# Kernel optimization log

Measured on AMD Instinct MI355X. Metric: run time of the kernel, lower is better.

## Reference

```python
import jax, jax.numpy as jnp
import numpy as np

DIM = 768
HEADS = 12
HIDDEN = 4 * DIM
EPS = 1e-5


def _layernorm(x, g, b):
    mu = jnp.mean(x, axis=-1, keepdims=True)
    var = jnp.var(x, axis=-1, keepdims=True)
    return (x - mu) * jax.lax.rsqrt(var + EPS) * g + b


def setup_inputs() -> dict:
    key = jax.random.key(0)
    ks = jax.random.split(key, 8)
    B, N, C = 16, 577, DIM
    s = lambda fan: 1.0 / np.sqrt(fan)
    return {
        "x": jax.random.normal(ks[0], (B, N, C), jnp.float32),
        "ln1_g": jnp.ones((C,), jnp.float32),
        "ln1_b": jnp.zeros((C,), jnp.float32),
        "qkv_w": jax.random.normal(ks[1], (C, 3 * C), jnp.float32) * s(C),
        "qkv_b": jnp.zeros((3 * C,), jnp.float32),
        "proj_w": jax.random.normal(ks[2], (C, C), jnp.float32) * s(C),
        "proj_b": jnp.zeros((C,), jnp.float32),
        "ln2_g": jnp.ones((C,), jnp.float32),
        "ln2_b": jnp.zeros((C,), jnp.float32),
        "fc1_w": jax.random.normal(ks[3], (C, HIDDEN), jnp.float32) * s(C),
        "fc1_b": jnp.zeros((HIDDEN,), jnp.float32),
        "fc2_w": jax.random.normal(ks[4], (HIDDEN, C), jnp.float32) * s(HIDDEN),
        "fc2_b": jnp.zeros((C,), jnp.float32),
    }


def reference(x, ln1_g, ln1_b, qkv_w, qkv_b, proj_w, proj_b,
              ln2_g, ln2_b, fc1_w, fc1_b, fc2_w, fc2_b):
    B, N, C = x.shape
    H = HEADS
    Dh = C // H
    scale = Dh ** (-0.5)

    # --- attention branch (pre-norm) ---
    xn = _layernorm(x, ln1_g, ln1_b)
    qkv = xn @ qkv_w + qkv_b                         # [B,N,3C]
    qkv = qkv.reshape(B, N, 3, H, Dh).transpose(2, 0, 3, 1, 4)  # [3,B,H,N,Dh]
    q, k, v = qkv[0], qkv[1], qkv[2]
    attn = jax.nn.softmax(jnp.einsum('bhnd,bhmd->bhnm', q, k) * scale, axis=-1)
    y = jnp.einsum('bhnm,bhmd->bhnd', attn, v)       # [B,H,N,Dh]
    y = y.transpose(0, 2, 1, 3).reshape(B, N, C)
    y = y @ proj_w + proj_b
    x = x + y

    # --- MLP branch (pre-norm, exact GELU as torch default) ---
    xn2 = _layernorm(x, ln2_g, ln2_b)
    h = jax.nn.gelu(xn2 @ fc1_w + fc1_b, approximate=False)
    x = x + (h @ fc2_w + fc2_b)
    return x
```

## Files before the change

### kernel.cpp

```cpp
#include <hip/hip_runtime.h>
#include <hip/hip_bf16.h>
#include <math.h>


#define C_DIM   768
#define SEQ     577
#define BATCH   16
#define NHEAD   12
#define DHEAD   64
#define MREAL   (BATCH*SEQ)
#define MPAD    9344
#define HID     3072
#define QKW     1536
#define NKV     640
#define QSCALE  0.1803368801111204f

typedef __hip_bfloat16 bf16;
typedef __attribute__((ext_vector_type(8))) short v8s;
typedef __attribute__((ext_vector_type(4))) float v4f;

static __device__ __forceinline__ bf16 f2b(float f){ return __float2bfloat16(f); }
static __device__ __forceinline__ float us2f(unsigned short u){
  union{ float f; unsigned int i; } x; x.i = ((unsigned int)u)<<16; return x.f;
}
static __device__ __forceinline__ short f2s(float f){
  bf16 t = __float2bfloat16(f); return *(short*)&t;
}
static __device__ __forceinline__ float gelu_fast(float x){
  float z2 = 2.302585092994046f * x * (1.f + 0.044715f*x*x);
  return x / (1.f + exp2f(-z2));
}


__global__ __launch_bounds__(256) void k_transpose_cast(
    const float* __restrict__ src, bf16* __restrict__ dst, int R, int C)
{
  __shared__ float s[64][65];
  const int tr = blockIdx.x*64, tc = blockIdx.y*64;
  const int t = threadIdx.x;
  const int lr = t >> 4, lc4 = t & 15;
  #pragma unroll
  for (int i=0;i<4;i++){
    int r = lr + i*16;
    float4 v = *(const float4*)(src + (size_t)(tr+r)*C + tc + lc4*4);
    s[r][lc4*4+0]=v.x; s[r][lc4*4+1]=v.y; s[r][lc4*4+2]=v.z; s[r][lc4*4+3]=v.w;
  }
  __syncthreads();
  const int c = t >> 2, seg = t & 3;
  alignas(16) bf16 tmp[16];
  #pragma unroll
  for (int j=0;j<16;j++) tmp[j] = f2b(s[seg*16+j][c]);
  bf16* dp = dst + (size_t)(tc+c)*R + tr + seg*16;
  *(uint4*)dp       = *(uint4*)tmp;
  *(uint4*)(dp + 8) = *(uint4*)(tmp + 8);
}

__global__ __launch_bounds__(256) void k_zero_pad(bf16* __restrict__ y)
{
  size_t i = (size_t)blockIdx.x*256 + threadIdx.x;
  y[(size_t)MREAL*C_DIM + i] = f2b(0.f);
}

__global__ __launch_bounds__(256) void k_layernorm(
    const float* __restrict__ in, const float* __restrict__ g,
    const float* __restrict__ b, bf16* __restrict__ o)
{
  int row = blockIdx.x, tid = threadIdx.x;
  size_t base = (size_t)row*C_DIM;
  if (row >= MREAL){
    #pragma unroll
    for (int j=0;j<3;j++) o[base + tid + j*256] = f2b(0.f);
    return;
  }
  float v[3], s=0.f, ss=0.f;
  #pragma unroll
  for (int j=0;j<3;j++){ v[j] = in[base + tid + j*256]; s += v[j]; ss += v[j]*v[j]; }
  #pragma unroll
  for (int off=32; off>0; off>>=1){ s += __shfl_xor(s,off); ss += __shfl_xor(ss,off); }
  __shared__ float red[8];
  int wv = tid>>6;
  if ((tid&63)==0){ red[wv] = s; red[4+wv] = ss; }
  __syncthreads();
  float S  = red[0]+red[1]+red[2]+red[3];
  float SS = red[4]+red[5]+red[6]+red[7];
  float mu   = S*(1.f/C_DIM);
  float rstd = rsqrtf(SS*(1.f/C_DIM) - mu*mu + 1e-5f);
  #pragma unroll
  for (int j=0;j<3;j++){
    int c = tid + j*256;
    o[base+c] = f2b((v[j]-mu)*rstd*g[c] + b[c]);
  }
}

__global__ __launch_bounds__(256) void k_reduce2(
    const bf16* __restrict__ P, const float* __restrict__ bias,
    float* __restrict__ out)
{
  size_t i = ((size_t)blockIdx.x*256 + threadIdx.x)*8;
  int c = (int)(i % C_DIM);
  v8s p0 = *(const v8s*)(P + i);
  v8s p1 = *(const v8s*)(P + (size_t)MPAD*C_DIM + i);
  float r[8];
  #pragma unroll
  for (int j=0;j<8;j++) r[j] = out[i+j];
  #pragma unroll
  for (int j=0;j<8;j++)
    out[i+j] = us2f((unsigned short)p0[j]) + us2f((unsigned short)p1[j])
             + bias[c+j] + r[j];
}

__global__ __launch_bounds__(256, 3) void k_flash(
    const bf16* __restrict__ qk, const bf16* __restrict__ VtAll,
    bf16* __restrict__ y)
{
  __shared__ alignas(16) bf16 sK[2][64*64];
  __shared__ alignas(16) bf16 sV[2][64*64];
  __shared__ alignas(16) bf16 sP[4][16*72];

  const int tid = threadIdx.x;
  const int wave = tid>>6, lane = tid&63;
  const int r16 = lane&15, kg = lane>>4;

  const int id = blockIdx.x;
  const int swz = (id&7)*240 + (id>>3);
  const int hh = swz/10, qt = swz - hh*10;
  const int b_ = hh/NHEAD, h_ = hh - b_*NHEAD;

  const int qrow = b_*SEQ + qt*64 + wave*16 + r16;
  v8s qf[2];
  qf[0] = *(const v8s*)(qk + (size_t)qrow*QKW + h_*DHEAD + kg*8);
  qf[1] = *(const v8s*)(qk + (size_t)qrow*QKW + h_*DHEAD + 32 + kg*8);

  auto stage = [&](int kt, int buf){
    #pragma unroll
    for (int i=0;i<2;i++){
      int chunk = i*256 + tid;
      int row = chunk>>3, ch = chunk&7;
      int sc = ch ^ (row&7);
      const bf16* gk = qk + (size_t)(b_*SEQ + kt*64 + row)*QKW
                          + C_DIM + h_*DHEAD + sc*8;
      const bf16* gv = VtAll + (size_t)(b_*C_DIM + h_*DHEAD + row)*NKV
                             + kt*64 + sc*8;
      __builtin_amdgcn_global_load_lds(
          (const __attribute__((address_space(1))) void*)gk,
          (__attribute__((address_space(3))) void*)((char*)&sK[buf][0] + i*4096 + wave*1024),
          16, 0, 0);
      __builtin_amdgcn_global_load_lds(
          (const __attribute__((address_space(1))) void*)gv,
          (__attribute__((address_space(3))) void*)((char*)&sV[buf][0] + i*4096 + wave*1024),
          16, 0, 0);
    }
  };

  float m_run = -1e30f, l_run = 0.f;
  v4f zero4 = {0.f,0.f,0.f,0.f};
  v4f o[4] = {zero4, zero4, zero4, zero4};

  stage(0, 0);
  for (int kt=0; kt<10; ++kt){
    __syncthreads();
    if (kt < 9) stage(kt+1, (kt+1)&1);
    const bf16* Kt = &sK[kt&1][0];
    const bf16* Vt = &sV[kt&1][0];

    v4f sfr[4] = {zero4, zero4, zero4, zero4};
    #pragma unroll
    for (int ks=0; ks<2; ++ks){
      #pragma unroll
      for (int m=0;m<4;m++){
        int key = m*16 + r16;
        v8s kf = *(const v8s*)(Kt + key*64 + (((ks*4+kg) ^ (key&7))*8));
        sfr[m] = __builtin_amdgcn_mfma_f32_16x16x32_bf16(kf, qf[ks], sfr[m], 0, 0, 0);
      }
    }

    if (kt == 9){
      #pragma unroll
      for (int m=0;m<4;m++)
        #pragma unroll
        for (int gg=0; gg<4; ++gg){
          int kb = 576 + m*16 + kg*4 + gg;
          if (kb >= SEQ) sfr[m][gg] = -1e30f;
        }
    }

    float tmax = -1e30f;
    #pragma unroll
    for (int m=0;m<4;m++)
      #pragma unroll
      for (int gg=0; gg<4; ++gg) tmax = fmaxf(tmax, sfr[m][gg]);
    tmax = fmaxf(tmax, __shfl_xor(tmax, 16));
    tmax = fmaxf(tmax, __shfl_xor(tmax, 32));
    float mn  = fmaxf(m_run, tmax);
    float scl = exp2f(m_run - mn);
    float ps  = 0.f;
    #pragma unroll
    for (int m=0;m<4;m++)
      #pragma unroll
      for (int gg=0; gg<4; ++gg){
        float pv = exp2f(sfr[m][gg] - mn);
        sfr[m][gg] = pv; ps += pv;
      }
    ps += __shfl_xor(ps, 16);
    ps += __shfl_xor(ps, 32);
    l_run = l_run*scl + ps;
    m_run = mn;
    #pragma unroll
    for (int mf=0; mf<4; ++mf) o[mf] *= scl;

    bf16* Pw = &sP[wave][0];
    #pragma unroll
    for (int m=0;m<4;m++){
      short4 w;
      w.x = f2s(sfr[m][0]); w.y = f2s(sfr[m][1]);
      w.z = f2s(sfr[m][2]); w.w = f2s(sfr[m][3]);
      *(short4*)(Pw + r16*72 + m*16 + kg*4) = w;
    }
    asm volatile("s_waitcnt lgkmcnt(0)" ::: "memory");
    v8s pb0 = *(const v8s*)(Pw + r16*72 + kg*8);
    v8s pb1 = *(const v8s*)(Pw + r16*72 + 32 + kg*8);
    #pragma unroll
    for (int mf=0; mf<4; ++mf){
      int d = mf*16 + r16;
      v8s v0 = *(const v8s*)(Vt + d*64 + ((kg     ^ (d&7))*8));
      v8s v1 = *(const v8s*)(Vt + d*64 + (((4+kg) ^ (d&7))*8));
      o[mf] = __builtin_amdgcn_mfma_f32_16x16x32_bf16(v0, pb0, o[mf], 0, 0, 0);
      o[mf] = __builtin_amdgcn_mfma_f32_16x16x32_bf16(v1, pb1, o[mf], 0, 0, 0);
    }
  }

  const int qg = qt*64 + wave*16 + r16;
  if (qg < SEQ){
    float inv = 1.f / l_run;
    #pragma unroll
    for (int mf=0; mf<4; ++mf){
      short4 w;
      w.x = f2s(o[mf][0]*inv); w.y = f2s(o[mf][1]*inv);
      w.z = f2s(o[mf][2]*inv); w.w = f2s(o[mf][3]*inv);
      *(short4*)(y + (size_t)(b_*SEQ + qg)*C_DIM + h_*DHEAD + mf*16 + kg*4) = w;
    }
  }
}

template<int EPI>
__global__ __launch_bounds__(256, 4) void gemm_bt(
    const bf16* __restrict__ A, int lda,
    const bf16* __restrict__ BT, int ldb,
    void* Cv, int ldc,
    const float* __restrict__ bias,
    const float* resid,
    int K)
{
  __shared__ alignas(16) bf16 sA[128*64];
  __shared__ alignas(16) bf16 sB[128*64];
  const int tid  = threadIdx.x;
  const int wave = tid>>6, lane = tid&63;
  const int wr = wave>>1, wc = wave&1;
  const int r16 = lane&15, kg = lane>>4;

  int nx = gridDim.x, nwg = nx*gridDim.y;
  int id = blockIdx.y*nx + blockIdx.x;
  int qq = nwg>>3, r8 = nwg&7, xcd = id&7, j = id>>3;
  int swz = (xcd<r8 ? xcd*(qq+1) : r8*(qq+1) + (xcd-r8)*qq) + j;
  int mt = swz / nx, nt = swz % nx;

  int kb = 0;
  if constexpr (EPI==6) kb = blockIdx.z * K;

  v4f acc[4][4];
  v4f zero4 = {0.f,0.f,0.f,0.f};
  #pragma unroll
  for (int m=0;m<4;m++)
    #pragma unroll
    for (int n=0;n<4;n++) acc[m][n] = zero4;

  const int mrow0 = mt*128, ncol0 = nt*128;

  for (int kt=0; kt<K; kt+=64){
    #pragma unroll
    for (int i=0;i<4;i++){
      int ci = wave*4 + i;
      int q  = ci*64 + lane;
      int rr = q>>3;
      int cc = (q&7)*8;
      const bf16* ga = A  + (size_t)(mrow0+rr)*lda + (kb+kt+cc);
      const bf16* gb = BT + (size_t)(ncol0+rr)*ldb + (kb+kt+cc);
      __builtin_amdgcn_global_load_lds(
          (const __attribute__((address_space(1))) void*)ga,
          (__attribute__((address_space(3))) void*)((char*)sA + ci*1024), 16, 0, 0);
      __builtin_amdgcn_global_load_lds(
          (const __attribute__((address_space(1))) void*)gb,
          (__attribute__((address_space(3))) void*)((char*)sB + ci*1024), 16, 0, 0);
    }
    __syncthreads();
    #pragma unroll
    for (int ks=0; ks<2; ks++){
      v8s av[4], bv[4];
      #pragma unroll
      for (int m=0;m<4;m++)
        av[m] = *(const v8s*)(sA + (wr*64 + m*16 + r16)*64 + ks*32 + kg*8);
      #pragma unroll
      for (int n=0;n<4;n++)
        bv[n] = *(const v8s*)(sB + (wc*64 + n*16 + r16)*64 + ks*32 + kg*8);
      #pragma unroll
      for (int m=0;m<4;m++)
        #pragma unroll
        for (int n=0;n<4;n++)
          acc[m][n] = __builtin_amdgcn_mfma_f32_16x16x32_bf16(av[m], bv[n], acc[m][n], 0, 0, 0);
    }
    __syncthreads();
  }

  #pragma unroll
  for (int m=0;m<4;m++){
    #pragma unroll
    for (int n=0;n<4;n++){
      int col = ncol0 + wc*64 + n*16 + r16;
      #pragma unroll
      for (int gg=0; gg<4; gg++){
        int row = mrow0 + wr*64 + m*16 + kg*4 + gg;
        float v = acc[m][n][gg];
        if constexpr (EPI==0){
          float oo = v + bias[col];
          if (col < C_DIM) oo *= QSCALE;
          ((bf16*)Cv)[(size_t)row*ldc + col] = f2b(oo);
        } else if constexpr (EPI==1){
          ((bf16*)Cv)[(size_t)row*ldc + col] = f2b(gelu_fast(v + bias[col]));
        } else if constexpr (EPI==2){
          if (row < MREAL){
            size_t idx = (size_t)row*ldc + col;
            ((float*)Cv)[idx] = v + bias[col] + resid[idx];
          }
        } else if constexpr (EPI==5){
          int g = col;
          if (g < MREAL){
            int b = g / SEQ;
            int key = g - b*SEQ;
            ((bf16*)Cv)[((size_t)b*C_DIM + row)*NKV + key] = f2b(v + bias[row]);
          }
        } else {
          ((bf16*)Cv)[(size_t)blockIdx.z*MPAD*C_DIM + (size_t)row*ldc + col] = f2b(v);
        }
      }
    }
  }
}


extern "C" void kernel_launch(void* const* d_in, const int* in_sizes, int n_in,
                              void* d_out, int out_size, void* d_ws, size_t ws_size,
                              hipStream_t stream)
{
  const float* x     = (const float*)d_in[0];
  const float* ln1g  = (const float*)d_in[1];
  const float* ln1b  = (const float*)d_in[2];
  const float* qkvw  = (const float*)d_in[3];
  const float* qkvb  = (const float*)d_in[4];
  const float* projw = (const float*)d_in[5];
  const float* projb = (const float*)d_in[6];
  const float* ln2g  = (const float*)d_in[7];
  const float* ln2b  = (const float*)d_in[8];
  const float* fc1w  = (const float*)d_in[9];
  const float* fc1b  = (const float*)d_in[10];
  const float* fc2w  = (const float*)d_in[11];
  const float* fc2b  = (const float*)d_in[12];
  float* out = (float*)d_out;

  char* p = (char*)d_ws;
  auto take = [&](size_t n){ char* r = p; p += (n + 255) & ~(size_t)255; return r; };
  bf16* qkvT = (bf16*)take((size_t)(3*C_DIM)*C_DIM*2);
  bf16* projT= (bf16*)take((size_t)C_DIM*C_DIM*2);
  bf16* fc1T = (bf16*)take((size_t)HID*C_DIM*2);
  bf16* fc2T = (bf16*)take((size_t)C_DIM*HID*2);
  bf16* xn   = (bf16*)take((size_t)MPAD*C_DIM*2);
  bf16* xn2  = (bf16*)take((size_t)MPAD*C_DIM*2);
  bf16* qk   = (bf16*)take((size_t)MPAD*QKW*2);
  bf16* y    = (bf16*)take((size_t)MPAD*C_DIM*2);
  bf16* h    = (bf16*)take((size_t)MPAD*HID*2);
  bf16* VtAll= (bf16*)take((size_t)(BATCH*C_DIM + 2*DHEAD)*NKV*2);
  bf16* P    = qk;

  k_transpose_cast<<<dim3(C_DIM/64, 3*C_DIM/64), 256, 0, stream>>>(qkvw, qkvT, C_DIM, 3*C_DIM);
  k_transpose_cast<<<dim3(C_DIM/64, C_DIM/64),  256, 0, stream>>>(projw, projT, C_DIM, C_DIM);
  k_transpose_cast<<<dim3(C_DIM/64, HID/64),    256, 0, stream>>>(fc1w, fc1T, C_DIM, HID);
  k_transpose_cast<<<dim3(HID/64,  C_DIM/64),   256, 0, stream>>>(fc2w, fc2T, HID, C_DIM);
  k_zero_pad<<<(MPAD-MREAL)*C_DIM/256, 256, 0, stream>>>(y);

  k_layernorm<<<MPAD, 256, 0, stream>>>(x, ln1g, ln1b, xn);

  gemm_bt<0><<<dim3(QKW/128, MPAD/128), 256, 0, stream>>>(
      xn, C_DIM, qkvT, C_DIM, qk, QKW, qkvb, nullptr, C_DIM);

  gemm_bt<5><<<dim3(MPAD/128, C_DIM/128), 256, 0, stream>>>(
      qkvT + (size_t)QKW*C_DIM, C_DIM, xn, C_DIM, VtAll, 0,
      qkvb + 2*C_DIM, nullptr, C_DIM);

  k_flash<<<1920, 256, 0, stream>>>(qk, VtAll, y);

  gemm_bt<2><<<dim3(C_DIM/128, MPAD/128), 256, 0, stream>>>(
      y, C_DIM, projT, C_DIM, out, C_DIM, projb, x, C_DIM);

  k_layernorm<<<MPAD, 256, 0, stream>>>(out, ln2g, ln2b, xn2);

  gemm_bt<1><<<dim3(HID/128, MPAD/128), 256, 0, stream>>>(
      xn2, C_DIM, fc1T, C_DIM, h, HID, fc1b, nullptr, C_DIM);

  gemm_bt<6><<<dim3(C_DIM/128, MPAD/128, 2), 256, 0, stream>>>(
      h, HID, fc2T, HID, P, C_DIM, nullptr, nullptr, HID/2);
  k_reduce2<<<(MREAL*C_DIM)/(256*8), 256, 0, stream>>>(P, fc2b, out);
}
```

Measured before the change: 314.5 us.

## Add 256x256 pipelined GEMM for fc1 and split-K the projection GEMM

Adds a new 512-thread GEMM kernel with 256x256 tiles that loads global memory directly into LDS, uses XOR-swizzled shared memory, an XCD-aware block remap and a four-phase schedule overlapping loads with MFMA. It replaces the fc1+GELU GEMM and is meant to raise data reuse and MFMA utilisation. The projection GEMM becomes a two-way split-K GEMM followed by a reduce kernel that adds bias and the residual, trading an extra partial-sum round trip through memory for more parallelism across 48 tiles. MPAD grows to 9472 so the row count divides by 256, which adds a little padded work to the other kernels.

```diff
diff --git a/kernel.cpp b/kernel.cpp
--- a/kernel.cpp
+++ b/kernel.cpp
@@ -9,7 +9,7 @@
 #define NHEAD   12
 #define DHEAD   64
 #define MREAL   (BATCH*SEQ)
-#define MPAD    9344
+#define MPAD    9472
 #define HID     3072
 #define QKW     1536
 #define NKV     640
@@ -94,7 +94,7 @@
 
 __global__ __launch_bounds__(256) void k_reduce2(
     const bf16* __restrict__ P, const float* __restrict__ bias,
-    float* __restrict__ out)
+    const float* __restrict__ resid, float* __restrict__ out)
 {
   size_t i = ((size_t)blockIdx.x*256 + threadIdx.x)*8;
   int c = (int)(i % C_DIM);
@@ -102,7 +102,7 @@
   v8s p1 = *(const v8s*)(P + (size_t)MPAD*C_DIM + i);
   float r[8];
   #pragma unroll
-  for (int j=0;j<8;j++) r[j] = out[i+j];
+  for (int j=0;j<8;j++) r[j] = resid[i+j];
   #pragma unroll
   for (int j=0;j<8;j++)
     out[i+j] = us2f((unsigned short)p0[j]) + us2f((unsigned short)p1[j])
@@ -324,13 +324,6 @@
           float oo = v + bias[col];
           if (col < C_DIM) oo *= QSCALE;
           ((bf16*)Cv)[(size_t)row*ldc + col] = f2b(oo);
-        } else if constexpr (EPI==1){
-          ((bf16*)Cv)[(size_t)row*ldc + col] = f2b(gelu_fast(v + bias[col]));
-        } else if constexpr (EPI==2){
-          if (row < MREAL){
-            size_t idx = (size_t)row*ldc + col;
-            ((float*)Cv)[idx] = v + bias[col] + resid[idx];
-          }
         } else if constexpr (EPI==5){
           int g = col;
           if (g < MREAL){
@@ -340,6 +333,183 @@
           }
         } else {
           ((bf16*)Cv)[(size_t)blockIdx.z*MPAD*C_DIM + (size_t)row*ldc + col] = f2b(v);
+        }
+      }
+    }
+  }
+}
+
+template<int EPI>
+__global__ __launch_bounds__(512, 2) void gemm256(
+    const bf16* __restrict__ A, int lda,
+    const bf16* __restrict__ BT, int ldb,
+    void* Cv, int ldc,
+    const float* __restrict__ bias,
+    int K)
+{
+  __shared__ bf16 sA[2][256*64];
+  __shared__ bf16 sB[2][256*64];
+  const int tid = threadIdx.x;
+  const int lane = tid & 63, wave = tid >> 6;
+  const int wm = wave >> 2, wn = wave & 3;
+  const int r16 = lane & 15, kg = lane >> 4;
+
+  int nx = gridDim.x, nwg = nx * gridDim.y;
+  int id = blockIdx.y * nx + blockIdx.x;
+  int qq = nwg >> 3, r8 = nwg & 7, xcd = id & 7, jj = id >> 3;
+  int swz = (xcd < r8 ? xcd*(qq+1) : r8*(qq+1) + (xcd-r8)*qq) + jj;
+  int mt = swz / nx, nt = swz % nx;
+  const int mrow0 = mt * 256, ncol0 = nt * 256;
+
+  const int srow   = tid >> 3;
+  const int schunk = (tid & 7) ^ (srow & 7);
+
+  const bf16* Ab = A  + (size_t)mrow0 * lda;
+  const bf16* Bb = BT + (size_t)ncol0 * ldb;
+
+  auto stA = [&](int T, int H){
+    #pragma unroll
+    for (int r = 0; r < 2; ++r){
+      const bf16* g = Ab + (size_t)(H*128 + r*64 + srow)*lda + (T*64 + schunk*8);
+      __builtin_amdgcn_global_load_lds(
+        (const __attribute__((address_space(1))) void*)g,
+        (__attribute__((address_space(3))) void*)((char*)&sA[T&1][0] + H*16384 + r*8192 + tid*16),
+        16, 0, 0);
+    }
+  };
+  auto stB = [&](int T, int H){
+    #pragma unroll
+    for (int r = 0; r < 2; ++r){
+      const bf16* g = Bb + (size_t)(H*128 + r*64 + srow)*ldb + (T*64 + schunk*8);
+      __builtin_amdgcn_global_load_lds(
+        (const __attribute__((address_space(1))) void*)g,
+        (__attribute__((address_space(3))) void*)((char*)&sB[T&1][0] + H*16384 + r*8192 + tid*16),
+        16, 0, 0);
+    }
+  };
+
+  v4f acc[8][4];
+  v4f zero4 = {0.f,0.f,0.f,0.f};
+  #pragma unroll
+  for (int m=0;m<8;m++)
+    #pragma unroll
+    for (int n=0;n<4;n++) acc[m][n] = zero4;
+
+  const int NK = K >> 6;
+
+  stA(0,0); stA(0,1); stB(0,0); stB(0,1); stB(1,0); stB(1,1);
+  asm volatile("s_waitcnt vmcnt(4)" ::: "memory");
+  asm volatile("s_barrier" ::: "memory");
+
+  v8s a0[4][2], a1[4][2], b0[2][2], b1[2][2];
+
+  for (int U = 0; U < NK; ++U){
+    const bf16* LA = &sA[U&1][0];
+    const bf16* LB = &sB[U&1][0];
+
+    #pragma unroll
+    for (int m=0;m<4;m++){
+      int row = wm*128 + m*16 + r16;
+      #pragma unroll
+      for (int ks=0;ks<2;ks++)
+        a0[m][ks] = *(const v8s*)(LA + row*64 + (((ks*4+kg) ^ (row&7))<<3));
+    }
+    #pragma unroll
+    for (int n=0;n<2;n++){
+      int row = wn*64 + n*16 + r16;
+      #pragma unroll
+      for (int ks=0;ks<2;ks++)
+        b0[n][ks] = *(const v8s*)(LB + row*64 + (((ks*4+kg) ^ (row&7))<<3));
+    }
+    if (U+1 < NK) stA(U+1, 0);
+    asm volatile("s_barrier" ::: "memory");
+    asm volatile("s_waitcnt lgkmcnt(0)" ::: "memory");
+    __builtin_amdgcn_sched_barrier(0);
+    __builtin_amdgcn_s_setprio(1);
+    #pragma unroll
+    for (int m=0;m<4;m++)
+      #pragma unroll
+      for (int n=0;n<2;n++)
+        #pragma unroll
+        for (int ks=0;ks<2;ks++)
+          acc[m][n] = __builtin_amdgcn_mfma_f32_16x16x32_bf16(a0[m][ks], b0[n][ks], acc[m][n], 0,0,0);
+    __builtin_amdgcn_s_setprio(0);
+    asm volatile("s_barrier" ::: "memory");
+
+    #pragma unroll
+    for (int n=0;n<2;n++){
+      int row = wn*64 + (n+2)*16 + r16;
+      #pragma unroll
+      for (int ks=0;ks<2;ks++)
+        b1[n][ks] = *(const v8s*)(LB + row*64 + (((ks*4+kg) ^ (row&7))<<3));
+    }
+    if (U+1 < NK) stA(U+1, 1);
+    asm volatile("s_barrier" ::: "memory");
+    asm volatile("s_waitcnt lgkmcnt(0)" ::: "memory");
+    __builtin_amdgcn_sched_barrier(0);
+    __builtin_amdgcn_s_setprio(1);
+    #pragma unroll
+    for (int m=0;m<4;m++)
+      #pragma unroll
+      for (int n=0;n<2;n++)
+        #pragma unroll
+        for (int ks=0;ks<2;ks++)
+          acc[m][n+2] = __builtin_amdgcn_mfma_f32_16x16x32_bf16(a0[m][ks], b1[n][ks], acc[m][n+2], 0,0,0);
+    __builtin_amdgcn_s_setprio(0);
+    asm volatile("s_barrier" ::: "memory");
+
+    #pragma unroll
+    for (int m=0;m<4;m++){
+      int row = wm*128 + (m+4)*16 + r16;
+      #pragma unroll
+      for (int ks=0;ks<2;ks++)
+        a1[m][ks] = *(const v8s*)(LA + row*64 + (((ks*4+kg) ^ (row&7))<<3));
+    }
+    if (U+2 < NK) stB(U+2, 0);
+    asm volatile("s_barrier" ::: "memory");
+    asm volatile("s_waitcnt lgkmcnt(0)" ::: "memory");
+    __builtin_amdgcn_sched_barrier(0);
+    __builtin_amdgcn_s_setprio(1);
+    #pragma unroll
+    for (int m=0;m<4;m++)
+      #pragma unroll
+      for (int n=0;n<2;n++)
+        #pragma unroll
+        for (int ks=0;ks<2;ks++)
+          acc[m+4][n] = __builtin_amdgcn_mfma_f32_16x16x32_bf16(a1[m][ks], b0[n][ks], acc[m+4][n], 0,0,0);
+    __builtin_amdgcn_s_setprio(0);
+    asm volatile("s_barrier" ::: "memory");
+
+    if (U+2 < NK){
+      stB(U+2, 1);
+      asm volatile("s_waitcnt vmcnt(4)" ::: "memory");
+    } else {
+      asm volatile("s_waitcnt vmcnt(0)" ::: "memory");
+    }
+    asm volatile("s_barrier" ::: "memory");
+    __builtin_amdgcn_s_setprio(1);
+    #pragma unroll
+    for (int m=0;m<4;m++)
+      #pragma unroll
+      for (int n=0;n<2;n++)
+        #pragma unroll
+        for (int ks=0;ks<2;ks++)
+          acc[m+4][n+2] = __builtin_amdgcn_mfma_f32_16x16x32_bf16(a1[m][ks], b1[n][ks], acc[m+4][n+2], 0,0,0);
+    __builtin_amdgcn_s_setprio(0);
+    asm volatile("s_barrier" ::: "memory");
+  }
+
+  #pragma unroll
+  for (int m=0;m<8;m++){
+    #pragma unroll
+    for (int n=0;n<4;n++){
+      int col = ncol0 + wn*64 + n*16 + r16;
+      #pragma unroll
+      for (int gg=0; gg<4; ++gg){
+        int row = mrow0 + wm*128 + m*16 + kg*4 + gg;
+        float v = acc[m][n][gg];
+        if constexpr (EPI==1){
+          ((bf16*)Cv)[(size_t)row*ldc + col] = f2b(gelu_fast(v + bias[col]));
         }
       }
     }
@@ -397,15 +567,16 @@
 
   k_flash<<<1920, 256, 0, stream>>>(qk, VtAll, y);
 
-  gemm_bt<2><<<dim3(C_DIM/128, MPAD/128), 256, 0, stream>>>(
-      y, C_DIM, projT, C_DIM, out, C_DIM, projb, x, C_DIM);
+  gemm_bt<6><<<dim3(C_DIM/128, MPAD/128, 2), 256, 0, stream>>>(
+      y, C_DIM, projT, C_DIM, P, C_DIM, nullptr, nullptr, C_DIM/2);
+  k_reduce2<<<(MREAL*C_DIM)/(256*8), 256, 0, stream>>>(P, projb, x, out);
 
   k_layernorm<<<MPAD, 256, 0, stream>>>(out, ln2g, ln2b, xn2);
 
-  gemm_bt<1><<<dim3(HID/128, MPAD/128), 256, 0, stream>>>(
-      xn2, C_DIM, fc1T, C_DIM, h, HID, fc1b, nullptr, C_DIM);
+  gemm256<1><<<dim3(HID/256, MPAD/256), 512, 0, stream>>>(
+      xn2, C_DIM, fc1T, C_DIM, h, HID, fc1b, C_DIM);
 
   gemm_bt<6><<<dim3(C_DIM/128, MPAD/128, 2), 256, 0, stream>>>(
       h, HID, fc2T, HID, P, C_DIM, nullptr, nullptr, HID/2);
-  k_reduce2<<<(MREAL*C_DIM)/(256*8), 256, 0, stream>>>(P, fc2b, out);
-}
+  k_reduce2<<<(MREAL*C_DIM)/(256*8), 256, 0, stream>>>(P, fc2b, out, out);
+}
```

New measurement: 316.7 us. About the same (+0.7%).

## Split-K the projection GEMM and fuse its reduction with the second LayerNorm

Applied to the files above, without the earlier changes.

The projection GEMM now runs as a two-way split-K into bf16 partial buffers, which doubles the number of workgroups for a grid that was small relative to the CU count. A new kernel sums the two partials, adds bias and residual, writes the fp32 output and applies LayerNorm 2 in the same pass, replacing the separate LayerNorm launch. The padding-zeroing kernel is dropped, MPAD grows by one 128-row tile, and the GEMM launch bound is raised to 5 blocks per CU. In exchange, the projection partial sums are rounded to bf16 before the residual add, and the extra partial writes and reads add memory traffic.

```diff
diff --git a/kernel.cpp b/kernel.cpp
--- a/kernel.cpp
+++ b/kernel.cpp
@@ -9,7 +9,7 @@
 #define NHEAD   12
 #define DHEAD   64
 #define MREAL   (BATCH*SEQ)
-#define MPAD    9344
+#define MPAD    9472
 #define HID     3072
 #define QKW     1536
 #define NKV     640
@@ -53,12 +53,6 @@
   bf16* dp = dst + (size_t)(tc+c)*R + tr + seg*16;
   *(uint4*)dp       = *(uint4*)tmp;
   *(uint4*)(dp + 8) = *(uint4*)(tmp + 8);
-}
-
-__global__ __launch_bounds__(256) void k_zero_pad(bf16* __restrict__ y)
-{
-  size_t i = (size_t)blockIdx.x*256 + threadIdx.x;
-  y[(size_t)MREAL*C_DIM + i] = f2b(0.f);
 }
 
 __global__ __launch_bounds__(256) void k_layernorm(
@@ -92,9 +86,49 @@
   }
 }
 
+__global__ __launch_bounds__(256) void k_reduce2_ln(
+    const bf16* __restrict__ P, const float* __restrict__ bias,
+    const float* __restrict__ resid, float* __restrict__ out,
+    const float* __restrict__ g, const float* __restrict__ bln,
+    bf16* __restrict__ xn2)
+{
+  int row = blockIdx.x, tid = threadIdx.x;
+  size_t base = (size_t)row*C_DIM;
+  if (row >= MREAL){
+    #pragma unroll
+    for (int j=0;j<3;j++) xn2[base + tid + j*256] = f2b(0.f);
+    return;
+  }
+  const unsigned short* P0 = (const unsigned short*)P;
+  const unsigned short* P1 = P0 + (size_t)MPAD*C_DIM;
+  float v[3], s=0.f, ss=0.f;
+  #pragma unroll
+  for (int j=0;j<3;j++){
+    int c = tid + j*256;
+    size_t idx = base + c;
+    float val = us2f(P0[idx]) + us2f(P1[idx]) + bias[c] + resid[idx];
+    out[idx] = val; v[j] = val; s += val; ss += val*val;
+  }
+  #pragma unroll
+  for (int off=32; off>0; off>>=1){ s += __shfl_xor(s,off); ss += __shfl_xor(ss,off); }
+  __shared__ float red[8];
+  int wv = tid>>6;
+  if ((tid&63)==0){ red[wv] = s; red[4+wv] = ss; }
+  __syncthreads();
+  float S  = red[0]+red[1]+red[2]+red[3];
+  float SS = red[4]+red[5]+red[6]+red[7];
+  float mu   = S*(1.f/C_DIM);
+  float rstd = rsqrtf(SS*(1.f/C_DIM) - mu*mu + 1e-5f);
+  #pragma unroll
+  for (int j=0;j<3;j++){
+    int c = tid + j*256;
+    xn2[base+c] = f2b((v[j]-mu)*rstd*g[c] + bln[c]);
+  }
+}
+
 __global__ __launch_bounds__(256) void k_reduce2(
     const bf16* __restrict__ P, const float* __restrict__ bias,
-    float* __restrict__ out)
+    const float* __restrict__ resid, float* __restrict__ out)
 {
   size_t i = ((size_t)blockIdx.x*256 + threadIdx.x)*8;
   int c = (int)(i % C_DIM);
@@ -102,7 +136,7 @@
   v8s p1 = *(const v8s*)(P + (size_t)MPAD*C_DIM + i);
   float r[8];
   #pragma unroll
-  for (int j=0;j<8;j++) r[j] = out[i+j];
+  for (int j=0;j<8;j++) r[j] = resid[i+j];
   #pragma unroll
   for (int j=0;j<8;j++)
     out[i+j] = us2f((unsigned short)p0[j]) + us2f((unsigned short)p1[j])
@@ -243,7 +277,7 @@
 }
 
 template<int EPI>
-__global__ __launch_bounds__(256, 4) void gemm_bt(
+__global__ __launch_bounds__(256, 5) void gemm_bt(
     const bf16* __restrict__ A, int lda,
     const bf16* __restrict__ BT, int ldb,
     void* Cv, int ldc,
@@ -326,11 +360,6 @@
           ((bf16*)Cv)[(size_t)row*ldc + col] = f2b(oo);
         } else if constexpr (EPI==1){
           ((bf16*)Cv)[(size_t)row*ldc + col] = f2b(gelu_fast(v + bias[col]));
-        } else if constexpr (EPI==2){
-          if (row < MREAL){
-            size_t idx = (size_t)row*ldc + col;
-            ((float*)Cv)[idx] = v + bias[col] + resid[idx];
-          }
         } else if constexpr (EPI==5){
           int g = col;
           if (g < MREAL){
@@ -384,7 +413,6 @@
   k_transpose_cast<<<dim3(C_DIM/64, C_DIM/64),  256, 0, stream>>>(projw, projT, C_DIM, C_DIM);
   k_transpose_cast<<<dim3(C_DIM/64, HID/64),    256, 0, stream>>>(fc1w, fc1T, C_DIM, HID);
   k_transpose_cast<<<dim3(HID/64,  C_DIM/64),   256, 0, stream>>>(fc2w, fc2T, HID, C_DIM);
-  k_zero_pad<<<(MPAD-MREAL)*C_DIM/256, 256, 0, stream>>>(y);
 
   k_layernorm<<<MPAD, 256, 0, stream>>>(x, ln1g, ln1b, xn);
 
@@ -397,15 +425,14 @@
 
   k_flash<<<1920, 256, 0, stream>>>(qk, VtAll, y);
 
-  gemm_bt<2><<<dim3(C_DIM/128, MPAD/128), 256, 0, stream>>>(
-      y, C_DIM, projT, C_DIM, out, C_DIM, projb, x, C_DIM);
-
-  k_layernorm<<<MPAD, 256, 0, stream>>>(out, ln2g, ln2b, xn2);
+  gemm_bt<6><<<dim3(C_DIM/128, MPAD/128, 2), 256, 0, stream>>>(
+      y, C_DIM, projT, C_DIM, P, C_DIM, nullptr, nullptr, C_DIM/2);
+  k_reduce2_ln<<<MPAD, 256, 0, stream>>>(P, projb, x, out, ln2g, ln2b, xn2);
 
   gemm_bt<1><<<dim3(HID/128, MPAD/128), 256, 0, stream>>>(
       xn2, C_DIM, fc1T, C_DIM, h, HID, fc1b, nullptr, C_DIM);
 
   gemm_bt<6><<<dim3(C_DIM/128, MPAD/128, 2), 256, 0, stream>>>(
       h, HID, fc2T, HID, P, C_DIM, nullptr, nullptr, HID/2);
-  k_reduce2<<<(MREAL*C_DIM)/(256*8), 256, 0, stream>>>(P, fc2b, out);
-}
+  k_reduce2<<<(MREAL*C_DIM)/(256*8), 256, 0, stream>>>(P, fc2b, out, out);
+}
```

Measured after the change: 458.0 us. 45.7% more time.
